# Kernel optimization log

Measured on AMD Instinct MI355X. Metric: run time of the kernel, lower is better.

The kernel has to match this reference:

```python
import jax, jax.numpy as jnp
import numpy as np

# Mamba2(d_model=256, headdim=32) defaults: d_state=128, d_conv=4, expand=2, ngroups=1, chunk=256
B, CIN, L = 8, 256, 1024
D_MODEL = CIN
D_INNER = 2 * D_MODEL            # expand=2 -> 512
HEADDIM = 32
NHEADS = D_INNER // HEADDIM      # 16
D_STATE = 128
D_CONV = 4
CONV_DIM = D_INNER + 2 * D_STATE             # 768 (ngroups=1)
D_IN_PROJ = 2 * D_INNER + 2 * D_STATE + NHEADS  # 1296
GN_GROUPS = 8
CHUNK = 256
EPS = 1e-5

def setup_inputs():
    key = jax.random.key(0)
    ks = jax.random.split(key, 8)
    x = jax.random.normal(ks[0], (B, CIN, L), jnp.float32)
    W_in = jax.random.normal(ks[1], (D_IN_PROJ, D_MODEL), jnp.float32) * 0.02
    conv_w = jax.random.normal(ks[2], (CONV_DIM, D_CONV), jnp.float32) * 0.2
    conv_b = jax.random.normal(ks[3], (CONV_DIM,), jnp.float32) * 0.02
    dt = jnp.exp(jax.random.uniform(ks[4], (NHEADS,)) * (jnp.log(0.1) - jnp.log(0.001)) + jnp.log(0.001))
    dt_bias = dt + jnp.log(-jnp.expm1(-dt))   # inverse softplus
    A_log = jnp.log(jax.random.uniform(ks[5], (NHEADS,), minval=1.0, maxval=16.0))
    Dp = jnp.ones((NHEADS,), jnp.float32)
    rms_w = jnp.ones((D_INNER,), jnp.float32)
    W_out = jax.random.normal(ks[6], (D_MODEL, D_INNER), jnp.float32) * 0.02
    gn_w = jnp.ones((CIN,), jnp.float32)
    gn_b = jnp.zeros((CIN,), jnp.float32)
    return dict(x=x, W_in=W_in, conv_w=conv_w, conv_b=conv_b, dt_bias=dt_bias,
                A_log=A_log, Dp=Dp, rms_w=rms_w, W_out=W_out, gn_w=gn_w, gn_b=gn_b)

def segsum(a):
    # a: (..., T) -> (..., T, T) with sum_{j<i<=t} a_i on/below diagonal, -inf above
    T = a.shape[-1]
    cs = jnp.cumsum(a, -1)
    d = cs[..., :, None] - cs[..., None, :]
    mask = jnp.tril(jnp.ones((T, T), bool))
    return jnp.where(mask, d, -jnp.inf)

def ssd(X, A, Bm, Cm):
    # X: (b,l,h,p) already dt-scaled; A: (b,l,h) = dt*A_cont; Bm,Cm: (b,l,n) (ngroups=1)
    b, l, h, p = X.shape
    n = Bm.shape[-1]
    c = l // CHUNK
    X = X.reshape(b, c, CHUNK, h, p)
    A = A.reshape(b, c, CHUNK, h).transpose(0, 3, 1, 2)      # (b,h,c,l)
    Bm = Bm.reshape(b, c, CHUNK, n)
    Cm = Cm.reshape(b, c, CHUNK, n)
    A_cs = jnp.cumsum(A, -1)                                  # (b,h,c,l)
    Lmat = jnp.exp(segsum(A))                                 # (b,h,c,l,l)
    Y_diag = jnp.einsum('bcln,bcsn,bhcls,bcshp->bclhp', Cm, Bm, Lmat, X)
    decay_states = jnp.exp(A_cs[..., -1:] - A_cs)             # (b,h,c,l)
    states = jnp.einsum('bcln,bhcl,bclhp->bchpn', Bm, decay_states, X)
    decay_chunk = jnp.exp(segsum(jnp.pad(A_cs[..., -1], ((0, 0), (0, 0), (1, 0)))))  # (b,h,c+1,c+1)
    states = jnp.concatenate([jnp.zeros_like(states[:, :1]), states], axis=1)        # (b,c+1,h,p,n)
    prev = jnp.einsum('bhzc,bchpn->bzhpn', decay_chunk, states)[:, :-1]              # (b,c,h,p,n)
    Y_off = jnp.einsum('bcln,bchpn,bhcl->bclhp', Cm, prev, jnp.exp(A_cs))
    return (Y_diag + Y_off).reshape(b, l, h, p)

def _forward(x, W_in, conv_w, conv_b, dt_bias, A_log, Dp, rms_w, W_out, gn_w, gn_b):
    u = jnp.transpose(x, (0, 2, 1))                           # (B,L,d_model)
    zxbcdt = u @ W_in.T                                       # (B,L,1296)
    z = zxbcdt[..., :D_INNER]
    xBC = zxbcdt[..., D_INNER:D_INNER + CONV_DIM]
    dt = jax.nn.softplus(zxbcdt[..., D_INNER + CONV_DIM:] + dt_bias)  # (B,L,H)
    # causal depthwise conv1d + SiLU
    xpad = jnp.pad(xBC, ((0, 0), (D_CONV - 1, 0), (0, 0)))
    xconv = conv_b + sum(conv_w[:, k] * xpad[:, k:k + L, :] for k in range(D_CONV))
    xconv = jax.nn.silu(xconv)
    xs = xconv[..., :D_INNER].reshape(B, L, NHEADS, HEADDIM)
    Bm = xconv[..., D_INNER:D_INNER + D_STATE]
    Cm = xconv[..., D_INNER + D_STATE:]
    A = -jnp.exp(A_log)                                       # (H,)
    Y = ssd(dt[..., None] * xs, dt * A, Bm, Cm)               # (B,L,H,P)
    Y = Y + xs * Dp[None, None, :, None]
    # gated RMSNorm (norm_before_gate=False): rmsnorm(y * silu(z)) * weight
    y = Y.reshape(B, L, D_INNER) * jax.nn.silu(z)
    y = y * jax.lax.rsqrt(jnp.mean(y * y, -1, keepdims=True) + EPS) * rms_w
    out = jnp.transpose(y @ W_out.T, (0, 2, 1))               # (B,C,L)
    # GroupNorm(8, C) over (channels_per_group, L)
    og = out.reshape(B, GN_GROUPS, CIN // GN_GROUPS, L)
    mu = og.mean((2, 3), keepdims=True)
    var = og.var((2, 3), keepdims=True)
    out = ((og - mu) * jax.lax.rsqrt(var + EPS)).reshape(B, CIN, L)
    out = out * gn_w[None, :, None] + gn_b[None, :, None]
    return out * jnp.tanh(jax.nn.softplus(out))               # Mish

def reference(x, W_in, conv_w, conv_b, dt_bias, A_log, Dp, rms_w, W_out, gn_w, gn_b):
    return _forward(x, W_in, conv_w, conv_b, dt_bias, A_log, Dp, rms_w, W_out, gn_w, gn_b)
```

## Files before the change

### kernel.cpp

```cpp
#include <hip/hip_runtime.h>
#include <hip/hip_bf16.h>
#include <math.h>

#define B_ 8
#define L_ 1024
#define DM 256
#define DI 512
#define HD 32
#define NH 16
#define DS 128
#define CDIM 768
#define NZX 1280
#define CH 256
#define NC 4
#define M_ (B_*L_)
#define EPSV 1e-5f

typedef short bf16x8 __attribute__((ext_vector_type(8)));
typedef float f32x4 __attribute__((ext_vector_type(4)));

#define OFF_ZX   0
#define SZ_ZX    (M_*NZX/2)
#define OFF_XC   (OFF_ZX+SZ_ZX)
#define SZ_XC    (M_*CDIM/2)
#define OFF_DTP  (OFF_XC+SZ_XC)
#define SZ_DTP   (4*M_*NH)
#define OFF_ACS  (OFF_DTP+SZ_DTP)
#define SZ_ACS   (B_*NC*NH*CH)
#define OFF_S0   (OFF_ACS+SZ_ACS)
#define SZ_S0    (B_*NC*CH*CH/2)
#define OFF_ST   (OFF_S0+SZ_S0)
#define SZ_ST    (B_*NC*NH*HD*DS/2)
#define OFF_Y    (OFF_ST+SZ_ST)
#define SZ_Y     (M_*DI/2)
#define OFF_YNB  (OFF_Y+SZ_Y)
#define SZ_YNB   (M_*DI/2)
#define OFF_XBF  (OFF_YNB+SZ_YNB)
#define SZ_XBF   (M_*DM/2)
#define OFF_WBF  (OFF_XBF+SZ_XBF)
#define SZ_WBF   (1296*DM/2)
#define OFF_WOBF (OFF_WBF+SZ_WBF)
#define SZ_WOBF  (DM*DI/2)
#define OFF_GNP  (OFF_WOBF+SZ_WOBF)
#define SZ_GNP   (64*2)
#define OFF_BT   (OFF_GNP+SZ_GNP)
#define SZ_BT    (32*128*256/2)
#define OFF_OUTB (OFF_BT+SZ_BT)
#define SZ_OUTB  (M_*DM/2)

__device__ __forceinline__ ushort f2bf(float v) {
  __hip_bfloat16 h = __float2bfloat16(v);
  return *(ushort*)&h;
}
__device__ __forceinline__ float bf2f(ushort u) {
  return __uint_as_float(((unsigned int)u) << 16);
}
__device__ __forceinline__ float dt_load(const float* __restrict__ dtp, size_t di) {
  float s = dtp[di] + dtp[(size_t)M_*NH + di] + dtp[2*(size_t)M_*NH + di] + dtp[3*(size_t)M_*NH + di];
  return (s > 20.f) ? s : log1pf(expf(s));
}

__device__ __forceinline__ void gload16(const ushort* g, ushort* l) {
  __builtin_amdgcn_global_load_lds(
      (const __attribute__((address_space(1))) unsigned int*)g,
      (__attribute__((address_space(3))) unsigned int*)l,
      16, 0, 0);
}

__global__ __launch_bounds__(256) void k_prep(const float* __restrict__ x,
                                              const float* __restrict__ W_in,
                                              const float* __restrict__ W_out,
                                              const float* __restrict__ dt_bias,
                                              ushort* __restrict__ xbf,
                                              ushort* __restrict__ wbf,
                                              ushort* __restrict__ wobf,
                                              float2* __restrict__ gnp,
                                              float* __restrict__ dtp) {
  __shared__ float Ts[64][65];
  __shared__ float Wd[16][65];
  const int bid = blockIdx.x;
  const int t = threadIdx.x;
  if (bid < 512) {
    const int kt = bid & 3, lt2 = (bid >> 2) & 15, b = bid >> 6;
    const int k0 = kt*64, l0 = lt2*64;
    for (int i = t; i < 1024; i += 256) {
      int kk = i>>4, lw = i&15;
      float4 v = *(const float4*)&x[(size_t)b*DM*L_ + (size_t)(k0+kk)*L_ + l0 + lw*4];
      Ts[kk][lw*4+0] = v.x; Ts[kk][lw*4+1] = v.y;
      Ts[kk][lw*4+2] = v.z; Ts[kk][lw*4+3] = v.w;
    }
    for (int i = t; i < 1024; i += 256) {
      int h = i>>6, kk = i&63;
      Wd[h][kk] = W_in[(size_t)(NZX+h)*DM + k0+kk];
    }
    __syncthreads();
    for (int i = t; i < 512; i += 256) {
      int mm = i>>3, kg = i&7;
      union { ushort u[8]; uint4 q; } pk;
#pragma unroll
      for (int j = 0; j < 8; ++j) pk.u[j] = f2bf(Ts[kg*8+j][mm]);
      *(uint4*)&xbf[(size_t)(b*L_ + l0+mm)*DM + k0 + kg*8] = pk.q;
    }
    const int h = t&15, lg = t>>4;
    const float bias = (kt == 0) ? dt_bias[h] : 0.f;
#pragma unroll
    for (int c = 0; c < 4; ++c) {
      const int ll = lg + c*16;
      float acc = bias;
#pragma unroll 8
      for (int kk = 0; kk < 64; ++kk) acc += Wd[h][kk]*Ts[kk][ll];
      dtp[(size_t)kt*M_*NH + (size_t)(b*L_ + l0+ll)*NH + h] = acc;
    }
  } else if (bid < 512 + 1296) {
    int i = (bid-512)*256 + t;
    if (i < 1296*DM) wbf[i] = f2bf(W_in[i]);
  } else if (bid < 512 + 1296 + 512) {
    int i = (bid-512-1296)*256 + t;
    wobf[i] = f2bf(W_out[i]);
  } else {
    if (t < 64) gnp[t] = make_float2(0.f, 0.f);
  }
}

__global__ __launch_bounds__(256) void k_gemm_in_mfma(const ushort* __restrict__ xbf,
                                                      const ushort* __restrict__ wbf,
                                                      ushort* __restrict__ zxb) {
  __shared__ __attribute__((aligned(16))) ushort As[2][128*32];
  __shared__ __attribute__((aligned(16))) ushort Bs[2][128*32];
  const int tid = threadIdx.x;
  const int n0 = blockIdx.x*128, m0 = blockIdx.y*128;
  const int wave = tid>>6, lane = tid&63;
  const int lr = lane&15, quad = lane>>4;
  const int rA = lane>>2;
  const int cA = (lane&3)*8;
  f32x4 acc[2][8];
#pragma unroll
  for (int mi=0;mi<2;++mi)
#pragma unroll
    for (int ni=0;ni<8;++ni)
#pragma unroll
      for (int r=0;r<4;++r) acc[mi][ni][r] = 0.f;
  auto STAGE = [&](int buf, int k0) {
#pragma unroll
    for (int j = 0; j < 2; ++j) {
      const int ch = 2*wave + j;
      const int row = ch*16 + rA;
      gload16(xbf + (size_t)(m0+row)*DM + k0 + cA, &As[buf][ch*512]);
      gload16(wbf + (size_t)(n0+row)*DM + k0 + cA, &Bs[buf][ch*512]);
    }
  };
  STAGE(0, 0);
#pragma unroll
  for (int i = 0; i < 8; ++i) {
    __syncthreads();
    if (i < 7) STAGE((i+1)&1, (i+1)*32);
    const int cur = i&1;
    bf16x8 af[2], bfr[8];
    af[0] = *(const bf16x8*)&As[cur][(wave*32+lr)*32 + quad*8];
    af[1] = *(const bf16x8*)&As[cur][(wave*32+16+lr)*32 + quad*8];
#pragma unroll
    for (int ni=0;ni<8;++ni) bfr[ni] = *(const bf16x8*)&Bs[cur][(ni*16+lr)*32 + quad*8];
#pragma unroll
    for (int mi=0;mi<2;++mi)
#pragma unroll
      for (int ni=0;ni<8;++ni)
        acc[mi][ni] = __builtin_amdgcn_mfma_f32_16x16x32_bf16(af[mi], bfr[ni], acc[mi][ni], 0, 0, 0);
  }
#pragma unroll
  for (int mi=0;mi<2;++mi) {
    int m = m0 + wave*32 + mi*16 + quad*4;
#pragma unroll
    for (int ni=0;ni<8;++ni) {
      int n = n0 + ni*16 + lr;
#pragma unroll
      for (int r=0;r<4;++r) zxb[(size_t)(m+r)*NZX + n] = f2bf(acc[mi][ni][r]);
    }
  }
}

__global__ __launch_bounds__(256) void k_conv(const ushort* __restrict__ zxb,
                                              const float* __restrict__ cw,
                                              const float* __restrict__ cb,
                                              ushort* __restrict__ xcb,
                                              ushort* __restrict__ btg) {
  const int j = blockIdx.x*256 + threadIdx.x;
  const int m8 = blockIdx.y*8;
  const int l0 = m8 & 1023;
  const int mb = m8 & ~1023;
  const float4 w = *(const float4*)&cw[j*4];
  const float bias = cb[j];
  float v[11];
#pragma unroll
  for (int i = 0; i < 11; ++i) {
    int ll = l0 - 3 + i;
    v[i] = (ll >= 0) ? bf2f(zxb[(size_t)(mb+ll)*NZX + DI + j]) : 0.f;
  }
  union { ushort u[8]; uint4 q; } res;
#pragma unroll
  for (int i = 0; i < 8; ++i) {
    float a = bias + w.x*v[i] + w.y*v[i+1] + w.z*v[i+2] + w.w*v[i+3];
    a = a / (1.f + expf(-a));
    res.u[i] = f2bf(a);
    xcb[(size_t)(mb+l0+i)*CDIM + j] = res.u[i];
  }
  if (j >= DI && j < DI+DS) {
    const int n = j - DI;
    const int bc = (mb >> 10)*NC + (l0 >> 8);
    const int lc = l0 & 255;
    *(uint4*)&btg[((size_t)bc*DS + n)*CH + lc] = res.q;
  }
}

__global__ __launch_bounds__(256) void k_s0st(const ushort* __restrict__ xcb,
                                              const ushort* __restrict__ btg,
                                              const float* __restrict__ dtp,
                                              const float* __restrict__ A_log,
                                              float* __restrict__ acs_g,
                                              ushort* __restrict__ stb,
                                              ushort* __restrict__ S0b) {
  __shared__ float wtot[4];
  __shared__ ushort Xw[32][264];
  const int role = blockIdx.x;
  const int bc = blockIdx.y;
  const int base = bc*CH;
  const int t = threadIdx.x;
  const int wave = t>>6, lane = t&63, lr = lane&15, quad = lane>>4;
  if (role < 10) {
    const int lt = (role>=6) ? 3 : (role>=3) ? 2 : (role>=1) ? 1 : 0;
    const int st = role - lt*(lt+1)/2;
    const int l = lt*64 + wave*16 + lr;
    f32x4 acc[4];
#pragma unroll
    for (int nt = 0; nt < 4; ++nt)
#pragma unroll
      for (int r = 0; r < 4; ++r) acc[nt][r] = 0.f;
#pragma unroll
    for (int ks = 0; ks < 4; ++ks) {
      bf16x8 af = *(const bf16x8*)(xcb + (size_t)(base+l)*CDIM + (DI+DS) + ks*32 + quad*8);
#pragma unroll
      for (int nt = 0; nt < 4; ++nt) {
        bf16x8 bf = *(const bf16x8*)(xcb + (size_t)(base + st*64 + nt*16 + lr)*CDIM + DI + ks*32 + quad*8);
        acc[nt] = __builtin_amdgcn_mfma_f32_16x16x32_bf16(af, bf, acc[nt], 0, 0, 0);
      }
    }
    const bool diag = (lt == st);
#pragma unroll
    for (int nt = 0; nt < 4; ++nt)
#pragma unroll
      for (int r = 0; r < 4; ++r) {
        const int lrow = lt*64 + wave*16 + quad*4 + r;
        const int scol = st*64 + nt*16 + lr;
        ushort v = (!diag || scol <= lrow) ? f2bf(acc[nt][r]) : (ushort)0;
        S0b[((size_t)bc*CH + lrow)*CH + scol] = v;
      }
    return;
  }
  const int h = role - 10;
  float dt_t = dt_load(dtp, (size_t)(base+t)*NH + h);
  float An = -expf(A_log[h]);
  float v = dt_t * An;
#pragma unroll
  for (int off = 1; off < 64; off <<= 1) {
    float u = __shfl_up(v, off);
    if (lane >= off) v += u;
  }
  if (lane == 63) wtot[wave] = v;
  __syncthreads();
  float pre = 0.f, tot = 0.f;
#pragma unroll
  for (int wj = 0; wj < 4; ++wj) {
    float wv = wtot[wj];
    tot += wv;
    if (wj < wave) pre += wv;
  }
  const float a = v + pre;
  const float alast = tot;
  acs_g[((size_t)bc*NH + h)*CH + t] = a;
  float w = expf(alast - a) * dt_t;
  {
    const ushort* xp = xcb + (size_t)(base+t)*CDIM + h*HD;
    ushort tmp[32];
    *(uint4*)&tmp[0]  = *(const uint4*)(xp);
    *(uint4*)&tmp[8]  = *(const uint4*)(xp+8);
    *(uint4*)&tmp[16] = *(const uint4*)(xp+16);
    *(uint4*)&tmp[24] = *(const uint4*)(xp+24);
#pragma unroll
    for (int p = 0; p < 32; ++p) Xw[p][t] = f2bf(bf2f(tmp[p]) * w);
  }
  __syncthreads();
  f32x4 acc2[2][2];
#pragma unroll
  for (int mt=0;mt<2;++mt)
#pragma unroll
    for (int nt=0;nt<2;++nt)
#pragma unroll
      for (int r=0;r<4;++r) acc2[mt][nt][r] = 0.f;
  const ushort* bp = btg + (size_t)bc*DS*CH;
#pragma unroll
  for (int k0 = 0; k0 < CH; k0 += 32) {
    bf16x8 a0 = *(const bf16x8*)&Xw[lr][k0 + quad*8];
    bf16x8 a1 = *(const bf16x8*)&Xw[16+lr][k0 + quad*8];
    bf16x8 b0 = *(const bf16x8*)(bp + (size_t)(wave*32 + lr)*CH + k0 + quad*8);
    bf16x8 b1 = *(const bf16x8*)(bp + (size_t)(wave*32 + 16 + lr)*CH + k0 + quad*8);
    acc2[0][0] = __builtin_amdgcn_mfma_f32_16x16x32_bf16(a0, b0, acc2[0][0], 0,0,0);
    acc2[0][1] = __builtin_amdgcn_mfma_f32_16x16x32_bf16(a0, b1, acc2[0][1], 0,0,0);
    acc2[1][0] = __builtin_amdgcn_mfma_f32_16x16x32_bf16(a1, b0, acc2[1][0], 0,0,0);
    acc2[1][1] = __builtin_amdgcn_mfma_f32_16x16x32_bf16(a1, b1, acc2[1][1], 0,0,0);
  }
  size_t sb = ((size_t)bc*NH + h)*HD*DS;
#pragma unroll
  for (int mt = 0; mt < 2; ++mt)
#pragma unroll
    for (int nt = 0; nt < 2; ++nt)
#pragma unroll
      for (int r = 0; r < 4; ++r)
        stb[sb + (size_t)(mt*16 + quad*4 + r)*DS + wave*32 + nt*16 + lr] = f2bf(acc2[mt][nt][r]);
}

__global__ __launch_bounds__(256) void k_y_mfma(const ushort* __restrict__ xcb,
    const float* __restrict__ dtp, const float* __restrict__ acs_g,
    const ushort* __restrict__ S0b, const ushort* __restrict__ stb,
    const float* __restrict__ Dp, ushort* __restrict__ Yb) {
  __shared__ ushort Xt[32][280];
  __shared__ ushort Xs[32][280];
  __shared__ float acs[CH];
  const int t = threadIdx.x;
  const int bc = blockIdx.x, h = blockIdx.y;
  const int base = bc*CH;
  const int cc = bc & 3, bc4 = bc & ~3;
  acs[t] = acs_g[((size_t)bc*NH + h)*CH + t];
  const float dts_t = dt_load(dtp, (size_t)(base+t)*NH + h);
  ushort tmp[32];
  {
    const ushort* xp = xcb + (size_t)(base+t)*CDIM + h*HD;
    *(uint4*)&tmp[0]  = *(const uint4*)(xp);
    *(uint4*)&tmp[8]  = *(const uint4*)(xp+8);
    *(uint4*)&tmp[16] = *(const uint4*)(xp+16);
    *(uint4*)&tmp[24] = *(const uint4*)(xp+24);
#pragma unroll
    for (int p = 0; p < 32; ++p) Xt[p][t] = tmp[p];
  }
  __syncthreads();
  const float e32 = expf(acs[t & ~31] - acs[t]) * dts_t;
#pragma unroll
  for (int p = 0; p < 32; ++p) Xs[p][t] = f2bf(bf2f(tmp[p]) * e32);
  __syncthreads();
  const int wave = t>>6, lane = t&63, lr = lane&15, quad = lane>>4;
  f32x4 acc[4][2];
#pragma unroll
  for (int mt=0;mt<4;++mt)
#pragma unroll
    for (int nt=0;nt<2;++nt)
#pragma unroll
      for (int r=0;r<4;++r) acc[mt][nt][r] = 0.f;
  if (cc > 0) {
    float fj[3];
    {
      float cum = 0.f;
      for (int j = cc-1; j >= 0; --j) {
        fj[j] = expf(cum);
        cum += acs_g[((size_t)(bc4+j)*NH + h)*CH + (CH-1)];
      }
    }
#pragma unroll
    for (int ks = 0; ks < 4; ++ks) {
      bf16x8 bfr[2];
#pragma unroll
      for (int nt = 0; nt < 2; ++nt) {
        float P[8];
#pragma unroll
        for (int jj = 0; jj < 8; ++jj) P[jj] = 0.f;
        for (int j = 0; j < cc; ++j) {
          bf16x8 sv = *(const bf16x8*)(stb + ((size_t)(bc4+j)*NH + h)*HD*DS
                                       + (size_t)(nt*16+lr)*DS + ks*32 + quad*8);
#pragma unroll
          for (int jj = 0; jj < 8; ++jj) P[jj] += fj[j]*bf2f((ushort)sv[jj]);
        }
        bf16x8 bb;
#pragma unroll
        for (int jj = 0; jj < 8; ++jj) bb[jj] = (short)f2bf(P[jj]);
        bfr[nt] = bb;
      }
#pragma unroll
      for (int mt = 0; mt < 4; ++mt) {
        int l = mt*64 + wave*16 + lr;
        bf16x8 af = *(const bf16x8*)(xcb + (size_t)(base+l)*CDIM + (DI+DS) + ks*32 + quad*8);
        acc[mt][0] = __builtin_amdgcn_mfma_f32_16x16x32_bf16(af, bfr[0], acc[mt][0], 0,0,0);
        acc[mt][1] = __builtin_amdgcn_mfma_f32_16x16x32_bf16(af, bfr[1], acc[mt][1], 0,0,0);
      }
    }
    const float es0 = expf(acs[0]);
#pragma unroll
    for (int mt = 0; mt < 4; ++mt)
#pragma unroll
      for (int nt = 0; nt < 2; ++nt)
#pragma unroll
        for (int r = 0; r < 4; ++r) acc[mt][nt][r] *= es0;
  }
  const int Kw = (12 + wave) >> 1;
  for (int ks = 0; ks <= Kw; ++ks) {
    const int sq = ks*32;
    const bf16x8 xb0 = *(const bf16x8*)&Xs[lr][sq + quad*8];
    const bf16x8 xb1 = *(const bf16x8*)&Xs[16+lr][sq + quad*8];
    const float g = (ks > 0) ? expf(acs[sq] - acs[sq-32]) : 1.f;
#pragma unroll
    for (int mt = 0; mt < 4; ++mt) {
      const int rt = 4*mt + wave;
      if (ks > (rt>>1)) continue;
      if (ks > 0) {
#pragma unroll
        for (int r = 0; r < 4; ++r) { acc[mt][0][r] *= g; acc[mt][1][r] *= g; }
      }
      const int l = mt*64 + wave*16 + lr;
      const bf16x8 sb = *(const bf16x8*)(S0b + ((size_t)bc*CH + l)*CH + sq + quad*8);
      acc[mt][0] = __builtin_amdgcn_mfma_f32_16x16x32_bf16(sb, xb0, acc[mt][0], 0,0,0);
      acc[mt][1] = __builtin_amdgcn_mfma_f32_16x16x32_bf16(sb, xb1, acc[mt][1], 0,0,0);
    }
  }
  const float dph = Dp[h];
#pragma unroll
  for (int mt = 0; mt < 4; ++mt) {
    const int Kmt = (4*mt + wave) >> 1;
    const float aref = acs[32*Kmt];
    const int lb = mt*64 + wave*16 + quad*4;
#pragma unroll
    for (int r = 0; r < 4; ++r) {
      const float e = expf(acs[lb+r] - aref);
#pragma unroll
      for (int nt = 0; nt < 2; ++nt) {
        const int p = nt*16 + lr;
        float xv = bf2f(Xt[p][lb+r]);
        Yb[(size_t)(base+lb+r)*DI + h*HD + p] = f2bf(acc[mt][nt][r]*e + dph*xv);
      }
    }
  }
}

__global__ __launch_bounds__(256) void k_rms(const ushort* __restrict__ zxb,
                                             const ushort* __restrict__ Yb,
                                             const float* __restrict__ rw,
                                             ushort* __restrict__ yn) {
  const int m = blockIdx.x*4 + (threadIdx.x>>6);
  const int lane = threadIdx.x & 63;
  const int c0 = lane*8;
  bf16x8 zv = *(const bf16x8*)(zxb + (size_t)m*NZX + c0);
  bf16x8 yv = *(const bf16x8*)(Yb  + (size_t)m*DI  + c0);
  float y[8];
  float ss = 0.f;
#pragma unroll
  for (int j = 0; j < 8; ++j) {
    float z = bf2f((ushort)zv[j]);
    y[j] = bf2f((ushort)yv[j]) * z / (1.f + expf(-z));
    ss += y[j]*y[j];
  }
#pragma unroll
  for (int off = 1; off < 64; off <<= 1) ss += __shfl_xor(ss, off);
  const float inv = rsqrtf(ss * (1.f/DI) + EPSV);
  float4 w0 = *(const float4*)&rw[c0];
  float4 w1 = *(const float4*)&rw[c0+4];
  const float wv[8] = {w0.x,w0.y,w0.z,w0.w,w1.x,w1.y,w1.z,w1.w};
  union { ushort u[8]; uint4 q; } pk;
#pragma unroll
  for (int j = 0; j < 8; ++j) pk.u[j] = f2bf(y[j] * inv * wv[j]);
  *(uint4*)(yn + (size_t)m*DI + c0) = pk.q;
}

__global__ __launch_bounds__(256) void k_gemm_out_mfma(const ushort* __restrict__ ynbf,
                                                       const ushort* __restrict__ wobf,
                                                       ushort* __restrict__ outb,
                                                       float2* __restrict__ gnp) {
  __shared__ __attribute__((aligned(16))) ushort As[2][64*64];
  __shared__ __attribute__((aligned(16))) ushort Bs[2][64*64];
  const int tid = threadIdx.x;
  const int n0 = blockIdx.x*64, m0 = blockIdx.y*64;
  const int wave = tid>>6, lane = tid&63;
  const int lr = lane&15, quad = lane>>4;
  const int rA = lane>>3;
  const int cA = ((lane&7) ^ rA)*8;
  f32x4 acc[2][2];
#pragma unroll
  for (int mi=0;mi<2;++mi)
#pragma unroll
    for (int ni=0;ni<2;++ni)
#pragma unroll
      for (int r=0;r<4;++r) acc[mi][ni][r] = 0.f;
  auto STAGE = [&](int buf, int k0) {
#pragma unroll
    for (int j = 0; j < 2; ++j) {
      const int ch = 2*wave + j;
      const int row = ch*8 + rA;
      gload16(ynbf + (size_t)(m0+row)*DI + k0 + cA, &As[buf][ch*512]);
      gload16(wobf + (size_t)(n0+row)*DI + k0 + cA, &Bs[buf][ch*512]);
    }
  };
  STAGE(0, 0);
  const int mw = wave>>1, nw = wave&1;
#pragma unroll
  for (int i = 0; i < 8; ++i) {
    __syncthreads();
    if (i < 7) STAGE((i+1)&1, (i+1)*64);
    const int cur = i&1;
#pragma unroll
    for (int ks = 0; ks < 2; ++ks) {
      bf16x8 af[2], bfr[2];
#pragma unroll
      for (int mi = 0; mi < 2; ++mi) {
        const int R = mw*32 + mi*16 + lr;
        af[mi] = *(const bf16x8*)&As[cur][R*64 + (((ks*4+quad) ^ (R&7))*8)];
      }
#pragma unroll
      for (int ni = 0; ni < 2; ++ni) {
        const int R = nw*32 + ni*16 + lr;
        bfr[ni] = *(const bf16x8*)&Bs[cur][R*64 + (((ks*4+quad) ^ (R&7))*8)];
      }
#pragma unroll
      for (int mi=0;mi<2;++mi)
#pragma unroll
        for (int ni=0;ni<2;++ni)
          acc[mi][ni] = __builtin_amdgcn_mfma_f32_16x16x32_bf16(af[mi], bfr[ni], acc[mi][ni], 0, 0, 0);
    }
  }
  const int b = m0 >> 10, l0 = m0 & 1023;
  float sg = 0.f, sq2 = 0.f;
#pragma unroll
  for (int mi=0;mi<2;++mi)
#pragma unroll
    for (int ni=0;ni<2;++ni) {
      const int n = n0 + nw*32 + ni*16 + lr;
      union { ushort u[4]; uint2 q; } pk;
#pragma unroll
      for (int r=0;r<4;++r) {
        const float v = acc[mi][ni][r];
        pk.u[r] = f2bf(v);
        sg += v; sq2 += v*v;
      }
      *(uint2*)&outb[(size_t)b*DM*L_ + (size_t)n*L_ + l0 + mw*32 + mi*16 + quad*4] = pk.q;
    }
#pragma unroll
  for (int off = 32; off > 0; off >>= 1) {
    sg  += __shfl_down(sg,  off);
    sq2 += __shfl_down(sq2, off);
  }
  if (lane == 0) {
    const int gi = b*8 + (n0>>5) + nw;
    atomicAdd(&gnp[gi].x, sg);
    atomicAdd(&gnp[gi].y, sq2);
  }
}

__global__ __launch_bounds__(256) void k_gn_apply(const float2* __restrict__ gnp,
                                                  const float* __restrict__ gw,
                                                  const float* __restrict__ gb,
                                                  const ushort* __restrict__ ob,
                                                  float* __restrict__ o) {
  const int ch = blockIdx.x & 255, b = blockIdx.x >> 8;
  const int t = threadIdx.x;
  float2 p = gnp[b*8 + (ch>>5)];
  const float mean = p.x * (1.f/(32.f*L_));
  const float var  = p.y * (1.f/(32.f*L_)) - mean*mean;
  const float inv  = rsqrtf(var + EPSV);
  const float w = gw[ch], bb = gb[ch];
  size_t base = (size_t)blockIdx.x * L_;
  ushort4 v = *(const ushort4*)&ob[base + t*4];
  float r[4] = {bf2f(v.x), bf2f(v.y), bf2f(v.z), bf2f(v.w)};
#pragma unroll
  for (int j = 0; j < 4; ++j) {
    float u = (r[j] - mean) * inv * w + bb;
    float m;
    if (u > 15.f) m = u;
    else {
      float e = expf(u);
      float a = 1.f + e;
      float a2 = a*a;
      m = u * (a2 - 1.f) / (a2 + 1.f);
    }
    r[j] = m;
  }
  *(float4*)&o[base + t*4] = make_float4(r[0], r[1], r[2], r[3]);
}

extern "C" void kernel_launch(void* const* d_in, const int* in_sizes, int n_in,
                              void* d_out, int out_size, void* d_ws, size_t ws_size,
                              hipStream_t stream) {
  const float* x       = (const float*)d_in[0];
  const float* W_in    = (const float*)d_in[1];
  const float* conv_w  = (const float*)d_in[2];
  const float* conv_b  = (const float*)d_in[3];
  const float* dt_bias = (const float*)d_in[4];
  const float* A_log   = (const float*)d_in[5];
  const float* Dp      = (const float*)d_in[6];
  const float* rms_w   = (const float*)d_in[7];
  const float* W_out   = (const float*)d_in[8];
  const float* gn_w    = (const float*)d_in[9];
  const float* gn_b    = (const float*)d_in[10];
  float* out = (float*)d_out;
  float* ws  = (float*)d_ws;

  ushort* zxb   = (ushort*)(ws + OFF_ZX);
  ushort* xcb   = (ushort*)(ws + OFF_XC);
  float*  dtp   = ws + OFF_DTP;
  float*  acs   = ws + OFF_ACS;
  ushort* S0b   = (ushort*)(ws + OFF_S0);
  ushort* stb   = (ushort*)(ws + OFF_ST);
  ushort* Ybb   = (ushort*)(ws + OFF_Y);
  ushort* ynbf  = (ushort*)(ws + OFF_YNB);
  ushort* xbf   = (ushort*)(ws + OFF_XBF);
  ushort* wbf   = (ushort*)(ws + OFF_WBF);
  ushort* wobf  = (ushort*)(ws + OFF_WOBF);
  float2* gnp   = (float2*)(ws + OFF_GNP);
  ushort* btg   = (ushort*)(ws + OFF_BT);
  ushort* outb  = (ushort*)(ws + OFF_OUTB);

  k_prep         <<<dim3(512+1296+512+1), 256, 0, stream>>>(x, W_in, W_out, dt_bias,
                                                            xbf, wbf, wobf, gnp, dtp);
  k_gemm_in_mfma <<<dim3(NZX/128, M_/128), 256, 0, stream>>>(xbf, wbf, zxb);
  k_conv         <<<dim3(3, M_/8), 256, 0, stream>>>(zxb, conv_w, conv_b, xcb, btg);
  k_s0st         <<<dim3(26, B_*NC), 256, 0, stream>>>(xcb, btg, dtp, A_log, acs, stb, S0b);
  k_y_mfma       <<<dim3(B_*NC, NH), 256, 0, stream>>>(xcb, dtp, acs, S0b, stb, Dp, Ybb);
  k_rms          <<<dim3(M_/4), 256, 0, stream>>>(zxb, Ybb, rms_w, ynbf);
  k_gemm_out_mfma<<<dim3(DM/64, M_/64), 256, 0, stream>>>(ynbf, wobf, outb, gnp);
  k_gn_apply     <<<dim3(B_*DM), 256, 0, stream>>>(gnp, gn_w, gn_b, outb, out);
}
```

Before: 179.4 us.

## Fuse all stages into a persistent megakernel with grid-wide atomic barriers

Replaces the eight separate kernel launches with one persistent kernel of 256 blocks that loops over each stage's work items and separates stages with atomic-counter grid barriers, plus a tiny init kernel that zeroes the barrier counters and the GroupNorm accumulators. Shared memory becomes a union across stages. Weight conversion is also vectorized to 8 elements per thread. This targets launch overhead and the tail gaps between kernels, but the fixed grid may underuse the GPU in the large stages, and the barriers rely on all blocks being co-resident.

Measured after the change: 421.9 us. 135% more time.

```diff
diff --git a/kernel.cpp b/kernel.cpp
--- a/kernel.cpp
+++ b/kernel.cpp
@@ -15,6 +15,7 @@
 #define NC 4
 #define M_ (B_*L_)
 #define EPSV 1e-5f
+#define GRID 256
 
 typedef short bf16x8 __attribute__((ext_vector_type(8)));
 typedef float f32x4 __attribute__((ext_vector_type(4)));
@@ -47,6 +48,7 @@
 #define SZ_BT    (32*128*256/2)
 #define OFF_OUTB (OFF_BT+SZ_BT)
 #define SZ_OUTB  (M_*DM/2)
+#define OFF_BAR  (OFF_OUTB+SZ_OUTB)
 
 __device__ __forceinline__ ushort f2bf(float v) {
   __hip_bfloat16 h = __float2bfloat16(v);
@@ -59,7 +61,6 @@
   float s = dtp[di] + dtp[(size_t)M_*NH + di] + dtp[2*(size_t)M_*NH + di] + dtp[3*(size_t)M_*NH + di];
   return (s > 20.f) ? s : log1pf(expf(s));
 }
-
 __device__ __forceinline__ void gload16(const ushort* g, ushort* l) {
   __builtin_amdgcn_global_load_lds(
       (const __attribute__((address_space(1))) unsigned int*)g,
@@ -67,516 +68,519 @@
       16, 0, 0);
 }
 
-__global__ __launch_bounds__(256) void k_prep(const float* __restrict__ x,
-                                              const float* __restrict__ W_in,
-                                              const float* __restrict__ W_out,
-                                              const float* __restrict__ dt_bias,
-                                              ushort* __restrict__ xbf,
-                                              ushort* __restrict__ wbf,
-                                              ushort* __restrict__ wobf,
-                                              float2* __restrict__ gnp,
-                                              float* __restrict__ dtp) {
-  __shared__ float Ts[64][65];
-  __shared__ float Wd[16][65];
-  const int bid = blockIdx.x;
+__device__ __forceinline__ void gbar(int* ctr) {
+  __syncthreads();
+  if (threadIdx.x == 0) {
+    __hip_atomic_fetch_add(ctr, 1, __ATOMIC_ACQ_REL, __HIP_MEMORY_SCOPE_AGENT);
+    while (__hip_atomic_load(ctr, __ATOMIC_ACQUIRE, __HIP_MEMORY_SCOPE_AGENT) < GRID)
+      __builtin_amdgcn_s_sleep(2);
+  }
+  __syncthreads();
+}
+
+union SMem {
+  struct { float Ts[64][65]; float Wd[16][65]; } prep;
+  struct { ushort As[2][128*32]; ushort Bs[2][128*32]; } gin;
+  struct { float wtot[4]; ushort Xw[32][264]; } s0;
+  struct { ushort Xt[32][280]; ushort Xs[32][280]; float acs[CH]; } y;
+  struct { ushort As[2][64*64]; ushort Bs[2][64*64]; } gout;
+};
+
+__global__ __launch_bounds__(256) void k_init(float2* __restrict__ gnp, int* __restrict__ bar) {
   const int t = threadIdx.x;
-  if (bid < 512) {
-    const int kt = bid & 3, lt2 = (bid >> 2) & 15, b = bid >> 6;
-    const int k0 = kt*64, l0 = lt2*64;
-    for (int i = t; i < 1024; i += 256) {
-      int kk = i>>4, lw = i&15;
-      float4 v = *(const float4*)&x[(size_t)b*DM*L_ + (size_t)(k0+kk)*L_ + l0 + lw*4];
-      Ts[kk][lw*4+0] = v.x; Ts[kk][lw*4+1] = v.y;
-      Ts[kk][lw*4+2] = v.z; Ts[kk][lw*4+3] = v.w;
-    }
-    for (int i = t; i < 1024; i += 256) {
-      int h = i>>6, kk = i&63;
-      Wd[h][kk] = W_in[(size_t)(NZX+h)*DM + k0+kk];
-    }
-    __syncthreads();
-    for (int i = t; i < 512; i += 256) {
-      int mm = i>>3, kg = i&7;
-      union { ushort u[8]; uint4 q; } pk;
-#pragma unroll
-      for (int j = 0; j < 8; ++j) pk.u[j] = f2bf(Ts[kg*8+j][mm]);
-      *(uint4*)&xbf[(size_t)(b*L_ + l0+mm)*DM + k0 + kg*8] = pk.q;
-    }
-    const int h = t&15, lg = t>>4;
-    const float bias = (kt == 0) ? dt_bias[h] : 0.f;
-#pragma unroll
-    for (int c = 0; c < 4; ++c) {
-      const int ll = lg + c*16;
-      float acc = bias;
-#pragma unroll 8
-      for (int kk = 0; kk < 64; ++kk) acc += Wd[h][kk]*Ts[kk][ll];
-      dtp[(size_t)kt*M_*NH + (size_t)(b*L_ + l0+ll)*NH + h] = acc;
-    }
-  } else if (bid < 512 + 1296) {
-    int i = (bid-512)*256 + t;
-    if (i < 1296*DM) wbf[i] = f2bf(W_in[i]);
-  } else if (bid < 512 + 1296 + 512) {
-    int i = (bid-512-1296)*256 + t;
-    wobf[i] = f2bf(W_out[i]);
-  } else {
-    if (t < 64) gnp[t] = make_float2(0.f, 0.f);
-  }
-}
-
-__global__ __launch_bounds__(256) void k_gemm_in_mfma(const ushort* __restrict__ xbf,
-                                                      const ushort* __restrict__ wbf,
-                                                      ushort* __restrict__ zxb) {
-  __shared__ __attribute__((aligned(16))) ushort As[2][128*32];
-  __shared__ __attribute__((aligned(16))) ushort Bs[2][128*32];
-  const int tid = threadIdx.x;
-  const int n0 = blockIdx.x*128, m0 = blockIdx.y*128;
-  const int wave = tid>>6, lane = tid&63;
-  const int lr = lane&15, quad = lane>>4;
-  const int rA = lane>>2;
-  const int cA = (lane&3)*8;
-  f32x4 acc[2][8];
-#pragma unroll
-  for (int mi=0;mi<2;++mi)
-#pragma unroll
-    for (int ni=0;ni<8;++ni)
-#pragma unroll
-      for (int r=0;r<4;++r) acc[mi][ni][r] = 0.f;
-  auto STAGE = [&](int buf, int k0) {
-#pragma unroll
-    for (int j = 0; j < 2; ++j) {
-      const int ch = 2*wave + j;
-      const int row = ch*16 + rA;
-      gload16(xbf + (size_t)(m0+row)*DM + k0 + cA, &As[buf][ch*512]);
-      gload16(wbf + (size_t)(n0+row)*DM + k0 + cA, &Bs[buf][ch*512]);
-    }
-  };
-  STAGE(0, 0);
-#pragma unroll
-  for (int i = 0; i < 8; ++i) {
-    __syncthreads();
-    if (i < 7) STAGE((i+1)&1, (i+1)*32);
-    const int cur = i&1;
-    bf16x8 af[2], bfr[8];
-    af[0] = *(const bf16x8*)&As[cur][(wave*32+lr)*32 + quad*8];
-    af[1] = *(const bf16x8*)&As[cur][(wave*32+16+lr)*32 + quad*8];
-#pragma unroll
-    for (int ni=0;ni<8;++ni) bfr[ni] = *(const bf16x8*)&Bs[cur][(ni*16+lr)*32 + quad*8];
-#pragma unroll
-    for (int mi=0;mi<2;++mi)
-#pragma unroll
-      for (int ni=0;ni<8;++ni)
-        acc[mi][ni] = __builtin_amdgcn_mfma_f32_16x16x32_bf16(af[mi], bfr[ni], acc[mi][ni], 0, 0, 0);
-  }
-#pragma unroll
-  for (int mi=0;mi<2;++mi) {
-    int m = m0 + wave*32 + mi*16 + quad*4;
-#pragma unroll
-    for (int ni=0;ni<8;++ni) {
-      int n = n0 + ni*16 + lr;
-#pragma unroll
-      for (int r=0;r<4;++r) zxb[(size_t)(m+r)*NZX + n] = f2bf(acc[mi][ni][r]);
-    }
-  }
-}
-
-__global__ __launch_bounds__(256) void k_conv(const ushort* __restrict__ zxb,
-                                              const float* __restrict__ cw,
-                                              const float* __restrict__ cb,
-                                              ushort* __restrict__ xcb,
-                                              ushort* __restrict__ btg) {
-  const int j = blockIdx.x*256 + threadIdx.x;
-  const int m8 = blockIdx.y*8;
-  const int l0 = m8 & 1023;
-  const int mb = m8 & ~1023;
-  const float4 w = *(const float4*)&cw[j*4];
-  const float bias = cb[j];
-  float v[11];
-#pragma unroll
-  for (int i = 0; i < 11; ++i) {
-    int ll = l0 - 3 + i;
-    v[i] = (ll >= 0) ? bf2f(zxb[(size_t)(mb+ll)*NZX + DI + j]) : 0.f;
-  }
-  union { ushort u[8]; uint4 q; } res;
-#pragma unroll
-  for (int i = 0; i < 8; ++i) {
-    float a = bias + w.x*v[i] + w.y*v[i+1] + w.z*v[i+2] + w.w*v[i+3];
-    a = a / (1.f + expf(-a));
-    res.u[i] = f2bf(a);
-    xcb[(size_t)(mb+l0+i)*CDIM + j] = res.u[i];
-  }
-  if (j >= DI && j < DI+DS) {
-    const int n = j - DI;
-    const int bc = (mb >> 10)*NC + (l0 >> 8);
-    const int lc = l0 & 255;
-    *(uint4*)&btg[((size_t)bc*DS + n)*CH + lc] = res.q;
-  }
-}
-
-__global__ __launch_bounds__(256) void k_s0st(const ushort* __restrict__ xcb,
-                                              const ushort* __restrict__ btg,
-                                              const float* __restrict__ dtp,
-                                              const float* __restrict__ A_log,
-                                              float* __restrict__ acs_g,
-                                              ushort* __restrict__ stb,
-                                              ushort* __restrict__ S0b) {
-  __shared__ float wtot[4];
-  __shared__ ushort Xw[32][264];
-  const int role = blockIdx.x;
-  const int bc = blockIdx.y;
-  const int base = bc*CH;
+  if (t < 64) gnp[t] = make_float2(0.f, 0.f);
+  if (t < 8)  bar[t] = 0;
+}
+
+__global__ __launch_bounds__(256, 2) void k_mega(
+    const float* __restrict__ x, const float* __restrict__ W_in,
+    const float* __restrict__ conv_w, const float* __restrict__ conv_b,
+    const float* __restrict__ dt_bias, const float* __restrict__ A_log,
+    const float* __restrict__ Dp, const float* __restrict__ rms_w,
+    const float* __restrict__ W_out, const float* __restrict__ gn_w,
+    const float* __restrict__ gn_b, float* __restrict__ out,
+    ushort* __restrict__ xbf, ushort* __restrict__ wbf, ushort* __restrict__ wobf,
+    float2* __restrict__ gnp, float* __restrict__ dtp,
+    ushort* __restrict__ zxb, ushort* __restrict__ xcb, ushort* __restrict__ btg,
+    float* __restrict__ acs_g, ushort* __restrict__ S0b, ushort* __restrict__ stb,
+    ushort* __restrict__ Yb, ushort* __restrict__ ynbf, ushort* __restrict__ outb,
+    int* __restrict__ bar) {
+  __shared__ SMem sm;
   const int t = threadIdx.x;
   const int wave = t>>6, lane = t&63, lr = lane&15, quad = lane>>4;
-  if (role < 10) {
-    const int lt = (role>=6) ? 3 : (role>=3) ? 2 : (role>=1) ? 1 : 0;
-    const int st = role - lt*(lt+1)/2;
-    const int l = lt*64 + wave*16 + lr;
-    f32x4 acc[4];
-#pragma unroll
-    for (int nt = 0; nt < 4; ++nt)
-#pragma unroll
-      for (int r = 0; r < 4; ++r) acc[nt][r] = 0.f;
-#pragma unroll
-    for (int ks = 0; ks < 4; ++ks) {
-      bf16x8 af = *(const bf16x8*)(xcb + (size_t)(base+l)*CDIM + (DI+DS) + ks*32 + quad*8);
-#pragma unroll
-      for (int nt = 0; nt < 4; ++nt) {
-        bf16x8 bf = *(const bf16x8*)(xcb + (size_t)(base + st*64 + nt*16 + lr)*CDIM + DI + ks*32 + quad*8);
-        acc[nt] = __builtin_amdgcn_mfma_f32_16x16x32_bf16(af, bf, acc[nt], 0, 0, 0);
-      }
-    }
-    const bool diag = (lt == st);
-#pragma unroll
-    for (int nt = 0; nt < 4; ++nt)
+
+  for (int bid = blockIdx.x; bid < 738; bid += GRID) {
+    if (bid < 512) {
+      const int kt = bid & 3, lt2 = (bid >> 2) & 15, b = bid >> 6;
+      const int k0 = kt*64, l0 = lt2*64;
+      for (int i = t; i < 1024; i += 256) {
+        int kk = i>>4, lw = i&15;
+        float4 v = *(const float4*)&x[(size_t)b*DM*L_ + (size_t)(k0+kk)*L_ + l0 + lw*4];
+        sm.prep.Ts[kk][lw*4+0] = v.x; sm.prep.Ts[kk][lw*4+1] = v.y;
+        sm.prep.Ts[kk][lw*4+2] = v.z; sm.prep.Ts[kk][lw*4+3] = v.w;
+      }
+      for (int i = t; i < 1024; i += 256) {
+        int hh = i>>6, kk = i&63;
+        sm.prep.Wd[hh][kk] = W_in[(size_t)(NZX+hh)*DM + k0+kk];
+      }
+      __syncthreads();
+      for (int i = t; i < 512; i += 256) {
+        int mm = i>>3, kg = i&7;
+        union { ushort u[8]; uint4 q; } pk;
+#pragma unroll
+        for (int j = 0; j < 8; ++j) pk.u[j] = f2bf(sm.prep.Ts[kg*8+j][mm]);
+        *(uint4*)&xbf[(size_t)(b*L_ + l0+mm)*DM + k0 + kg*8] = pk.q;
+      }
+      const int hh = t&15, lg = t>>4;
+      const float bias = (kt == 0) ? dt_bias[hh] : 0.f;
+#pragma unroll
+      for (int c = 0; c < 4; ++c) {
+        const int ll = lg + c*16;
+        float acc = bias;
+#pragma unroll 8
+        for (int kk = 0; kk < 64; ++kk) acc += sm.prep.Wd[hh][kk]*sm.prep.Ts[kk][ll];
+        dtp[(size_t)kt*M_*NH + (size_t)(b*L_ + l0+ll)*NH + hh] = acc;
+      }
+    } else if (bid < 674) {
+      const int i = ((bid-512)*256 + t)*8;
+      float4 a = *(const float4*)&W_in[i];
+      float4 b4 = *(const float4*)&W_in[i+4];
+      union { ushort u[8]; uint4 q; } pk;
+      pk.u[0]=f2bf(a.x); pk.u[1]=f2bf(a.y); pk.u[2]=f2bf(a.z); pk.u[3]=f2bf(a.w);
+      pk.u[4]=f2bf(b4.x); pk.u[5]=f2bf(b4.y); pk.u[6]=f2bf(b4.z); pk.u[7]=f2bf(b4.w);
+      *(uint4*)&wbf[i] = pk.q;
+    } else {
+      const int i = ((bid-674)*256 + t)*8;
+      float4 a = *(const float4*)&W_out[i];
+      float4 b4 = *(const float4*)&W_out[i+4];
+      union { ushort u[8]; uint4 q; } pk;
+      pk.u[0]=f2bf(a.x); pk.u[1]=f2bf(a.y); pk.u[2]=f2bf(a.z); pk.u[3]=f2bf(a.w);
+      pk.u[4]=f2bf(b4.x); pk.u[5]=f2bf(b4.y); pk.u[6]=f2bf(b4.z); pk.u[7]=f2bf(b4.w);
+      *(uint4*)&wobf[i] = pk.q;
+    }
+    __syncthreads();
+  }
+  gbar(&bar[0]);
+
+  for (int bid = blockIdx.x; bid < 640; bid += GRID) {
+    const int n0 = (bid%10)*128, m0 = (bid/10)*128;
+    const int rA = lane>>2, cA = (lane&3)*8;
+    f32x4 acc[2][8];
+#pragma unroll
+    for (int mi=0;mi<2;++mi)
+#pragma unroll
+      for (int ni=0;ni<8;++ni)
+#pragma unroll
+        for (int r=0;r<4;++r) acc[mi][ni][r] = 0.f;
+    auto STAGE = [&](int buf, int k0) {
+#pragma unroll
+      for (int j = 0; j < 2; ++j) {
+        const int ch = 2*wave + j;
+        const int row = ch*16 + rA;
+        gload16(xbf + (size_t)(m0+row)*DM + k0 + cA, &sm.gin.As[buf][ch*512]);
+        gload16(wbf + (size_t)(n0+row)*DM + k0 + cA, &sm.gin.Bs[buf][ch*512]);
+      }
+    };
+    STAGE(0, 0);
+#pragma unroll
+    for (int i = 0; i < 8; ++i) {
+      __syncthreads();
+      if (i < 7) STAGE((i+1)&1, (i+1)*32);
+      const int cur = i&1;
+      bf16x8 af[2], bfr[8];
+      af[0] = *(const bf16x8*)&sm.gin.As[cur][(wave*32+lr)*32 + quad*8];
+      af[1] = *(const bf16x8*)&sm.gin.As[cur][(wave*32+16+lr)*32 + quad*8];
+#pragma unroll
+      for (int ni=0;ni<8;++ni) bfr[ni] = *(const bf16x8*)&sm.gin.Bs[cur][(ni*16+lr)*32 + quad*8];
+#pragma unroll
+      for (int mi=0;mi<2;++mi)
+#pragma unroll
+        for (int ni=0;ni<8;++ni)
+          acc[mi][ni] = __builtin_amdgcn_mfma_f32_16x16x32_bf16(af[mi], bfr[ni], acc[mi][ni], 0, 0, 0);
+    }
+#pragma unroll
+    for (int mi=0;mi<2;++mi) {
+      int m = m0 + wave*32 + mi*16 + quad*4;
+#pragma unroll
+      for (int ni=0;ni<8;++ni) {
+        int n = n0 + ni*16 + lr;
+#pragma unroll
+        for (int r=0;r<4;++r) zxb[(size_t)(m+r)*NZX + n] = f2bf(acc[mi][ni][r]);
+      }
+    }
+    __syncthreads();
+  }
+  gbar(&bar[1]);
+
+  for (int bid = blockIdx.x; bid < 3072; bid += GRID) {
+    const int j = (bid%3)*256 + t;
+    const int m8 = (bid/3)*8;
+    const int l0 = m8 & 1023;
+    const int mb = m8 & ~1023;
+    const float4 w = *(const float4*)&conv_w[j*4];
+    const float bias = conv_b[j];
+    float v[11];
+#pragma unroll
+    for (int i = 0; i < 11; ++i) {
+      int ll = l0 - 3 + i;
+      v[i] = (ll >= 0) ? bf2f(zxb[(size_t)(mb+ll)*NZX + DI + j]) : 0.f;
+    }
+    union { ushort u[8]; uint4 q; } res;
+#pragma unroll
+    for (int i = 0; i < 8; ++i) {
+      float a = bias + w.x*v[i] + w.y*v[i+1] + w.z*v[i+2] + w.w*v[i+3];
+      a = a / (1.f + expf(-a));
+      res.u[i] = f2bf(a);
+      xcb[(size_t)(mb+l0+i)*CDIM + j] = res.u[i];
+    }
+    if (j >= DI && j < DI+DS) {
+      const int n = j - DI;
+      const int bc = (mb >> 10)*NC + (l0 >> 8);
+      const int lc = l0 & 255;
+      *(uint4*)&btg[((size_t)bc*DS + n)*CH + lc] = res.q;
+    }
+  }
+  gbar(&bar[2]);
+
+  for (int bid = blockIdx.x; bid < 832; bid += GRID) {
+    const int role = bid % 26;
+    const int bc = bid / 26;
+    const int base = bc*CH;
+    if (role < 10) {
+      const int lt = (role>=6) ? 3 : (role>=3) ? 2 : (role>=1) ? 1 : 0;
+      const int st = role - lt*(lt+1)/2;
+      const int l = lt*64 + wave*16 + lr;
+      f32x4 acc[4];
+#pragma unroll
+      for (int nt = 0; nt < 4; ++nt)
+#pragma unroll
+        for (int r = 0; r < 4; ++r) acc[nt][r] = 0.f;
+#pragma unroll
+      for (int ks = 0; ks < 4; ++ks) {
+        bf16x8 af = *(const bf16x8*)(xcb + (size_t)(base+l)*CDIM + (DI+DS) + ks*32 + quad*8);
+#pragma unroll
+        for (int nt = 0; nt < 4; ++nt) {
+          bf16x8 bf = *(const bf16x8*)(xcb + (size_t)(base + st*64 + nt*16 + lr)*CDIM + DI + ks*32 + quad*8);
+          acc[nt] = __builtin_amdgcn_mfma_f32_16x16x32_bf16(af, bf, acc[nt], 0, 0, 0);
+        }
+      }
+      const bool diag = (lt == st);
+#pragma unroll
+      for (int nt = 0; nt < 4; ++nt)
+#pragma unroll
+        for (int r = 0; r < 4; ++r) {
+          const int lrow = lt*64 + wave*16 + quad*4 + r;
+          const int scol = st*64 + nt*16 + lr;
+          ushort v = (!diag || scol <= lrow) ? f2bf(acc[nt][r]) : (ushort)0;
+          S0b[((size_t)bc*CH + lrow)*CH + scol] = v;
+        }
+    } else {
+      const int h = role - 10;
+      float dt_t = dt_load(dtp, (size_t)(base+t)*NH + h);
+      float An = -expf(A_log[h]);
+      float v = dt_t * An;
+#pragma unroll
+      for (int off = 1; off < 64; off <<= 1) {
+        float u = __shfl_up(v, off);
+        if (lane >= off) v += u;
+      }
+      if (lane == 63) sm.s0.wtot[wave] = v;
+      __syncthreads();
+      float pre = 0.f, tot = 0.f;
+#pragma unroll
+      for (int wj = 0; wj < 4; ++wj) {
+        float wv = sm.s0.wtot[wj];
+        tot += wv;
+        if (wj < wave) pre += wv;
+      }
+      const float a = v + pre;
+      const float alast = tot;
+      acs_g[((size_t)bc*NH + h)*CH + t] = a;
+      float w = expf(alast - a) * dt_t;
+      {
+        const ushort* xp = xcb + (size_t)(base+t)*CDIM + h*HD;
+        ushort tmp[32];
+        *(uint4*)&tmp[0]  = *(const uint4*)(xp);
+        *(uint4*)&tmp[8]  = *(const uint4*)(xp+8);
+        *(uint4*)&tmp[16] = *(const uint4*)(xp+16);
+        *(uint4*)&tmp[24] = *(const uint4*)(xp+24);
+#pragma unroll
+        for (int p = 0; p < 32; ++p) sm.s0.Xw[p][t] = f2bf(bf2f(tmp[p]) * w);
+      }
+      __syncthreads();
+      f32x4 acc2[2][2];
+#pragma unroll
+      for (int mt=0;mt<2;++mt)
+#pragma unroll
+        for (int nt=0;nt<2;++nt)
+#pragma unroll
+          for (int r=0;r<4;++r) acc2[mt][nt][r] = 0.f;
+      const ushort* bp = btg + (size_t)bc*DS*CH;
+#pragma unroll
+      for (int k0 = 0; k0 < CH; k0 += 32) {
+        bf16x8 a0 = *(const bf16x8*)&sm.s0.Xw[lr][k0 + quad*8];
+        bf16x8 a1 = *(const bf16x8*)&sm.s0.Xw[16+lr][k0 + quad*8];
+        bf16x8 b0 = *(const bf16x8*)(bp + (size_t)(wave*32 + lr)*CH + k0 + quad*8);
+        bf16x8 b1 = *(const bf16x8*)(bp + (size_t)(wave*32 + 16 + lr)*CH + k0 + quad*8);
+        acc2[0][0] = __builtin_amdgcn_mfma_f32_16x16x32_bf16(a0, b0, acc2[0][0], 0,0,0);
+        acc2[0][1] = __builtin_amdgcn_mfma_f32_16x16x32_bf16(a0, b1, acc2[0][1], 0,0,0);
+        acc2[1][0] = __builtin_amdgcn_mfma_f32_16x16x32_bf16(a1, b0, acc2[1][0], 0,0,0);
+        acc2[1][1] = __builtin_amdgcn_mfma_f32_16x16x32_bf16(a1, b1, acc2[1][1], 0,0,0);
+      }
+      size_t sb = ((size_t)bc*NH + h)*HD*DS;
+#pragma unroll
+      for (int mt = 0; mt < 2; ++mt)
+#pragma unroll
+        for (int nt = 0; nt < 2; ++nt)
+#pragma unroll
+          for (int r = 0; r < 4; ++r)
+            stb[sb + (size_t)(mt*16 + quad*4 + r)*DS + wave*32 + nt*16 + lr] = f2bf(acc2[mt][nt][r]);
+    }
+    __syncthreads();
+  }
+  gbar(&bar[3]);
+
+  for (int bid = blockIdx.x; bid < 512; bid += GRID) {
+    const int bc = bid & 31, h = bid >> 5;
+    const int base = bc*CH;
+    const int cc = bc & 3, bc4 = bc & ~3;
+    sm.y.acs[t] = acs_g[((size_t)bc*NH + h)*CH + t];
+    const float dts_t = dt_load(dtp, (size_t)(base+t)*NH + h);
+    ushort tmp[32];
+    {
+      const ushort* xp = xcb + (size_t)(base+t)*CDIM + h*HD;
+      *(uint4*)&tmp[0]  = *(const uint4*)(xp);
+      *(uint4*)&tmp[8]  = *(const uint4*)(xp+8);
+      *(uint4*)&tmp[16] = *(const uint4*)(xp+16);
+      *(uint4*)&tmp[24] = *(const uint4*)(xp+24);
+#pragma unroll
+      for (int p = 0; p < 32; ++p) sm.y.Xt[p][t] = tmp[p];
+    }
+    __syncthreads();
+    const float e32 = expf(sm.y.acs[t & ~31] - sm.y.acs[t]) * dts_t;
+#pragma unroll
+    for (int p = 0; p < 32; ++p) sm.y.Xs[p][t] = f2bf(bf2f(tmp[p]) * e32);
+    __syncthreads();
+    f32x4 acc[4][2];
+#pragma unroll
+    for (int mt=0;mt<4;++mt)
+#pragma unroll
+      for (int nt=0;nt<2;++nt)
+#pragma unroll
+        for (int r=0;r<4;++r) acc[mt][nt][r] = 0.f;
+    if (cc > 0) {
+      float fj[3];
+      {
+        float cum = 0.f;
+        for (int j = cc-1; j >= 0; --j) {
+          fj[j] = expf(cum);
+          cum += acs_g[((size_t)(bc4+j)*NH + h)*CH + (CH-1)];
+        }
+      }
+#pragma unroll
+      for (int ks = 0; ks < 4; ++ks) {
+        bf16x8 bfr[2];
+#pragma unroll
+        for (int nt = 0; nt < 2; ++nt) {
+          float P[8];
+#pragma unroll
+          for (int jj = 0; jj < 8; ++jj) P[jj] = 0.f;
+          for (int j = 0; j < cc; ++j) {
+            bf16x8 sv = *(const bf16x8*)(stb + ((size_t)(bc4+j)*NH + h)*HD*DS
+                                         + (size_t)(nt*16+lr)*DS + ks*32 + quad*8);
+#pragma unroll
+            for (int jj = 0; jj < 8; ++jj) P[jj] += fj[j]*bf2f((ushort)sv[jj]);
+          }
+          bf16x8 bb;
+#pragma unroll
+          for (int jj = 0; jj < 8; ++jj) bb[jj] = (short)f2bf(P[jj]);
+          bfr[nt] = bb;
+        }
+#pragma unroll
+        for (int mt = 0; mt < 4; ++mt) {
+          int l = mt*64 + wave*16 + lr;
+          bf16x8 af = *(const bf16x8*)(xcb + (size_t)(base+l)*CDIM + (DI+DS) + ks*32 + quad*8);
+          acc[mt][0] = __builtin_amdgcn_mfma_f32_16x16x32_bf16(af, bfr[0], acc[mt][0], 0,0,0);
+          acc[mt][1] = __builtin_amdgcn_mfma_f32_16x16x32_bf16(af, bfr[1], acc[mt][1], 0,0,0);
+        }
+      }
+      const float es0 = expf(sm.y.acs[0]);
+#pragma unroll
+      for (int mt = 0; mt < 4; ++mt)
+#pragma unroll
+        for (int nt = 0; nt < 2; ++nt)
+#pragma unroll
+          for (int r = 0; r < 4; ++r) acc[mt][nt][r] *= es0;
+    }
+    const int Kw = (12 + wave) >> 1;
+    for (int ks = 0; ks <= Kw; ++ks) {
+      const int sq = ks*32;
+      const bf16x8 xb0 = *(const bf16x8*)&sm.y.Xs[lr][sq + quad*8];
+      const bf16x8 xb1 = *(const bf16x8*)&sm.y.Xs[16+lr][sq + quad*8];
+      const float g = (ks > 0) ? expf(sm.y.acs[sq] - sm.y.acs[sq-32]) : 1.f;
+#pragma unroll
+      for (int mt = 0; mt < 4; ++mt) {
+        const int rt = 4*mt + wave;
+        if (ks > (rt>>1)) continue;
+        if (ks > 0) {
+#pragma unroll
+          for (int r = 0; r < 4; ++r) { acc[mt][0][r] *= g; acc[mt][1][r] *= g; }
+        }
+        const int l = mt*64 + wave*16 + lr;
+        const bf16x8 sb = *(const bf16x8*)(S0b + ((size_t)bc*CH + l)*CH + sq + quad*8);
+        acc[mt][0] = __builtin_amdgcn_mfma_f32_16x16x32_bf16(sb, xb0, acc[mt][0], 0,0,0);
+        acc[mt][1] = __builtin_amdgcn_mfma_f32_16x16x32_bf16(sb, xb1, acc[mt][1], 0,0,0);
+      }
+    }
+    const float dph = Dp[h];
+#pragma unroll
+    for (int mt = 0; mt < 4; ++mt) {
+      const int Kmt = (4*mt + wave) >> 1;
+      const float aref = sm.y.acs[32*Kmt];
+      const int lb = mt*64 + wave*16 + quad*4;
 #pragma unroll
       for (int r = 0; r < 4; ++r) {
-        const int lrow = lt*64 + wave*16 + quad*4 + r;
-        const int scol = st*64 + nt*16 + lr;
-        ushort v = (!diag || scol <= lrow) ? f2bf(acc[nt][r]) : (ushort)0;
-        S0b[((size_t)bc*CH + lrow)*CH + scol] = v;
-      }
-    return;
-  }
-  const int h = role - 10;
-  float dt_t = dt_load(dtp, (size_t)(base+t)*NH + h);
-  float An = -expf(A_log[h]);
-  float v = dt_t * An;
-#pragma unroll
-  for (int off = 1; off < 64; off <<= 1) {
-    float u = __shfl_up(v, off);
-    if (lane >= off) v += u;
-  }
-  if (lane == 63) wtot[wave] = v;
-  __syncthreads();
-  float pre = 0.f, tot = 0.f;
-#pragma unroll
-  for (int wj = 0; wj < 4; ++wj) {
-    float wv = wtot[wj];
-    tot += wv;
-    if (wj < wave) pre += wv;
-  }
-  const float a = v + pre;
-  const float alast = tot;
-  acs_g[((size_t)bc*NH + h)*CH + t] = a;
-  float w = expf(alast - a) * dt_t;
-  {
-    const ushort* xp = xcb + (size_t)(base+t)*CDIM + h*HD;
-    ushort tmp[32];
-    *(uint4*)&tmp[0]  = *(const uint4*)(xp);
-    *(uint4*)&tmp[8]  = *(const uint4*)(xp+8);
-    *(uint4*)&tmp[16] = *(const uint4*)(xp+16);
-    *(uint4*)&tmp[24] = *(const uint4*)(xp+24);
-#pragma unroll
-    for (int p = 0; p < 32; ++p) Xw[p][t] = f2bf(bf2f(tmp[p]) * w);
-  }
-  __syncthreads();
-  f32x4 acc2[2][2];
-#pragma unroll
-  for (int mt=0;mt<2;++mt)
-#pragma unroll
-    for (int nt=0;nt<2;++nt)
-#pragma unroll
-      for (int r=0;r<4;++r) acc2[mt][nt][r] = 0.f;
-  const ushort* bp = btg + (size_t)bc*DS*CH;
-#pragma unroll
-  for (int k0 = 0; k0 < CH; k0 += 32) {
-    bf16x8 a0 = *(const bf16x8*)&Xw[lr][k0 + quad*8];
-    bf16x8 a1 = *(const bf16x8*)&Xw[16+lr][k0 + quad*8];
-    bf16x8 b0 = *(const bf16x8*)(bp + (size_t)(wave*32 + lr)*CH + k0 + quad*8);
-    bf16x8 b1 = *(const bf16x8*)(bp + (size_t)(wave*32 + 16 + lr)*CH + k0 + quad*8);
-    acc2[0][0] = __builtin_amdgcn_mfma_f32_16x16x32_bf16(a0, b0, acc2[0][0], 0,0,0);
-    acc2[0][1] = __builtin_amdgcn_mfma_f32_16x16x32_bf16(a0, b1, acc2[0][1], 0,0,0);
-    acc2[1][0] = __builtin_amdgcn_mfma_f32_16x16x32_bf16(a1, b0, acc2[1][0], 0,0,0);
-    acc2[1][1] = __builtin_amdgcn_mfma_f32_16x16x32_bf16(a1, b1, acc2[1][1], 0,0,0);
-  }
-  size_t sb = ((size_t)bc*NH + h)*HD*DS;
-#pragma unroll
-  for (int mt = 0; mt < 2; ++mt)
-#pragma unroll
-    for (int nt = 0; nt < 2; ++nt)
-#pragma unroll
-      for (int r = 0; r < 4; ++r)
-        stb[sb + (size_t)(mt*16 + quad*4 + r)*DS + wave*32 + nt*16 + lr] = f2bf(acc2[mt][nt][r]);
-}
-
-__global__ __launch_bounds__(256) void k_y_mfma(const ushort* __restrict__ xcb,
-    const float* __restrict__ dtp, const float* __restrict__ acs_g,
-    const ushort* __restrict__ S0b, const ushort* __restrict__ stb,
-    const float* __restrict__ Dp, ushort* __restrict__ Yb) {
-  __shared__ ushort Xt[32][280];
-  __shared__ ushort Xs[32][280];
-  __shared__ float acs[CH];
-  const int t = threadIdx.x;
-  const int bc = blockIdx.x, h = blockIdx.y;
-  const int base = bc*CH;
-  const int cc = bc & 3, bc4 = bc & ~3;
-  acs[t] = acs_g[((size_t)bc*NH + h)*CH + t];
-  const float dts_t = dt_load(dtp, (size_t)(base+t)*NH + h);
-  ushort tmp[32];
-  {
-    const ushort* xp = xcb + (size_t)(base+t)*CDIM + h*HD;
-    *(uint4*)&tmp[0]  = *(const uint4*)(xp);
-    *(uint4*)&tmp[8]  = *(const uint4*)(xp+8);
-    *(uint4*)&tmp[16] = *(const uint4*)(xp+16);
-    *(uint4*)&tmp[24] = *(const uint4*)(xp+24);
-#pragma unroll
-    for (int p = 0; p < 32; ++p) Xt[p][t] = tmp[p];
-  }
-  __syncthreads();
-  const float e32 = expf(acs[t & ~31] - acs[t]) * dts_t;
-#pragma unroll
-  for (int p = 0; p < 32; ++p) Xs[p][t] = f2bf(bf2f(tmp[p]) * e32);
-  __syncthreads();
-  const int wave = t>>6, lane = t&63, lr = lane&15, quad = lane>>4;
-  f32x4 acc[4][2];
-#pragma unroll
-  for (int mt=0;mt<4;++mt)
-#pragma unroll
-    for (int nt=0;nt<2;++nt)
-#pragma unroll
-      for (int r=0;r<4;++r) acc[mt][nt][r] = 0.f;
-  if (cc > 0) {
-    float fj[3];
-    {
-      float cum = 0.f;
-      for (int j = cc-1; j >= 0; --j) {
-        fj[j] = expf(cum);
-        cum += acs_g[((size_t)(bc4+j)*NH + h)*CH + (CH-1)];
-      }
-    }
-#pragma unroll
-    for (int ks = 0; ks < 4; ++ks) {
-      bf16x8 bfr[2];
-#pragma unroll
-      for (int nt = 0; nt < 2; ++nt) {
-        float P[8];
-#pragma unroll
-        for (int jj = 0; jj < 8; ++jj) P[jj] = 0.f;
-        for (int j = 0; j < cc; ++j) {
-          bf16x8 sv = *(const bf16x8*)(stb + ((size_t)(bc4+j)*NH + h)*HD*DS
-                                       + (size_t)(nt*16+lr)*DS + ks*32 + quad*8);
-#pragma unroll
-          for (int jj = 0; jj < 8; ++jj) P[jj] += fj[j]*bf2f((ushort)sv[jj]);
-        }
-        bf16x8 bb;
-#pragma unroll
-        for (int jj = 0; jj < 8; ++jj) bb[jj] = (short)f2bf(P[jj]);
-        bfr[nt] = bb;
-      }
-#pragma unroll
-      for (int mt = 0; mt < 4; ++mt) {
-        int l = mt*64 + wave*16 + lr;
-        bf16x8 af = *(const bf16x8*)(xcb + (size_t)(base+l)*CDIM + (DI+DS) + ks*32 + quad*8);
-        acc[mt][0] = __builtin_amdgcn_mfma_f32_16x16x32_bf16(af, bfr[0], acc[mt][0], 0,0,0);
-        acc[mt][1] = __builtin_amdgcn_mfma_f32_16x16x32_bf16(af, bfr[1], acc[mt][1], 0,0,0);
-      }
-    }
-    const float es0 = expf(acs[0]);
-#pragma unroll
-    for (int mt = 0; mt < 4; ++mt)
-#pragma unroll
-      for (int nt = 0; nt < 2; ++nt)
-#pragma unroll
-        for (int r = 0; r < 4; ++r) acc[mt][nt][r] *= es0;
-  }
-  const int Kw = (12 + wave) >> 1;
-  for (int ks = 0; ks <= Kw; ++ks) {
-    const int sq = ks*32;
-    const bf16x8 xb0 = *(const bf16x8*)&Xs[lr][sq + quad*8];
-    const bf16x8 xb1 = *(const bf16x8*)&Xs[16+lr][sq + quad*8];
-    const float g = (ks > 0) ? expf(acs[sq] - acs[sq-32]) : 1.f;
-#pragma unroll
-    for (int mt = 0; mt < 4; ++mt) {
-      const int rt = 4*mt + wave;
-      if (ks > (rt>>1)) continue;
-      if (ks > 0) {
-#pragma unroll
-        for (int r = 0; r < 4; ++r) { acc[mt][0][r] *= g; acc[mt][1][r] *= g; }
-      }
-      const int l = mt*64 + wave*16 + lr;
-      const bf16x8 sb = *(const bf16x8*)(S0b + ((size_t)bc*CH + l)*CH + sq + quad*8);
-      acc[mt][0] = __builtin_amdgcn_mfma_f32_16x16x32_bf16(sb, xb0, acc[mt][0], 0,0,0);
-      acc[mt][1] = __builtin_amdgcn_mfma_f32_16x16x32_bf16(sb, xb1, acc[mt][1], 0,0,0);
-    }
-  }
-  const float dph = Dp[h];
-#pragma unroll
-  for (int mt = 0; mt < 4; ++mt) {
-    const int Kmt = (4*mt + wave) >> 1;
-    const float aref = acs[32*Kmt];
-    const int lb = mt*64 + wave*16 + quad*4;
-#pragma unroll
-    for (int r = 0; r < 4; ++r) {
-      const float e = expf(acs[lb+r] - aref);
-#pragma unroll
-      for (int nt = 0; nt < 2; ++nt) {
-        const int p = nt*16 + lr;
-        float xv = bf2f(Xt[p][lb+r]);
-        Yb[(size_t)(base+lb+r)*DI + h*HD + p] = f2bf(acc[mt][nt][r]*e + dph*xv);
-      }
-    }
-  }
-}
-
-__global__ __launch_bounds__(256) void k_rms(const ushort* __restrict__ zxb,
-                                             const ushort* __restrict__ Yb,
-                                             const float* __restrict__ rw,
-                                             ushort* __restrict__ yn) {
-  const int m = blockIdx.x*4 + (threadIdx.x>>6);
-  const int lane = threadIdx.x & 63;
-  const int c0 = lane*8;
-  bf16x8 zv = *(const bf16x8*)(zxb + (size_t)m*NZX + c0);
-  bf16x8 yv = *(const bf16x8*)(Yb  + (size_t)m*DI  + c0);
-  float y[8];
-  float ss = 0.f;
-#pragma unroll
-  for (int j = 0; j < 8; ++j) {
-    float z = bf2f((ushort)zv[j]);
-    y[j] = bf2f((ushort)yv[j]) * z / (1.f + expf(-z));
-    ss += y[j]*y[j];
-  }
-#pragma unroll
-  for (int off = 1; off < 64; off <<= 1) ss += __shfl_xor(ss, off);
-  const float inv = rsqrtf(ss * (1.f/DI) + EPSV);
-  float4 w0 = *(const float4*)&rw[c0];
-  float4 w1 = *(const float4*)&rw[c0+4];
-  const float wv[8] = {w0.x,w0.y,w0.z,w0.w,w1.x,w1.y,w1.z,w1.w};
-  union { ushort u[8]; uint4 q; } pk;
-#pragma unroll
-  for (int j = 0; j < 8; ++j) pk.u[j] = f2bf(y[j] * inv * wv[j]);
-  *(uint4*)(yn + (size_t)m*DI + c0) = pk.q;
-}
-
-__global__ __launch_bounds__(256) void k_gemm_out_mfma(const ushort* __restrict__ ynbf,
-                                                       const ushort* __restrict__ wobf,
-                                                       ushort* __restrict__ outb,
-                                                       float2* __restrict__ gnp) {
-  __shared__ __attribute__((aligned(16))) ushort As[2][64*64];
-  __shared__ __attribute__((aligned(16))) ushort Bs[2][64*64];
-  const int tid = threadIdx.x;
-  const int n0 = blockIdx.x*64, m0 = blockIdx.y*64;
-  const int wave = tid>>6, lane = tid&63;
-  const int lr = lane&15, quad = lane>>4;
-  const int rA = lane>>3;
-  const int cA = ((lane&7) ^ rA)*8;
-  f32x4 acc[2][2];
-#pragma unroll
-  for (int mi=0;mi<2;++mi)
-#pragma unroll
-    for (int ni=0;ni<2;++ni)
-#pragma unroll
-      for (int r=0;r<4;++r) acc[mi][ni][r] = 0.f;
-  auto STAGE = [&](int buf, int k0) {
-#pragma unroll
-    for (int j = 0; j < 2; ++j) {
-      const int ch = 2*wave + j;
-      const int row = ch*8 + rA;
-      gload16(ynbf + (size_t)(m0+row)*DI + k0 + cA, &As[buf][ch*512]);
-      gload16(wobf + (size_t)(n0+row)*DI + k0 + cA, &Bs[buf][ch*512]);
-    }
-  };
-  STAGE(0, 0);
-  const int mw = wave>>1, nw = wave&1;
-#pragma unroll
-  for (int i = 0; i < 8; ++i) {
+        const float e = expf(sm.y.acs[lb+r] - aref);
+#pragma unroll
+        for (int nt = 0; nt < 2; ++nt) {
+          const int p = nt*16 + lr;
+          float xv = bf2f(sm.y.Xt[p][lb+r]);
+          Yb[(size_t)(base+lb+r)*DI + h*HD + p] = f2bf(acc[mt][nt][r]*e + dph*xv);
+        }
+      }
+    }
     __syncthreads();
-    if (i < 7) STAGE((i+1)&1, (i+1)*64);
-    const int cur = i&1;
-#pragma unroll
-    for (int ks = 0; ks < 2; ++ks) {
-      bf16x8 af[2], bfr[2];
-#pragma unroll
-      for (int mi = 0; mi < 2; ++mi) {
-        const int R = mw*32 + mi*16 + lr;
-        af[mi] = *(const bf16x8*)&As[cur][R*64 + (((ks*4+quad) ^ (R&7))*8)];
-      }
-#pragma unroll
-      for (int ni = 0; ni < 2; ++ni) {
-        const int R = nw*32 + ni*16 + lr;
-        bfr[ni] = *(const bf16x8*)&Bs[cur][R*64 + (((ks*4+quad) ^ (R&7))*8)];
-      }
-#pragma unroll
-      for (int mi=0;mi<2;++mi)
-#pragma unroll
-        for (int ni=0;ni<2;++ni)
-          acc[mi][ni] = __builtin_amdgcn_mfma_f32_16x16x32_bf16(af[mi], bfr[ni], acc[mi][ni], 0, 0, 0);
-    }
-  }
-  const int b = m0 >> 10, l0 = m0 & 1023;
-  float sg = 0.f, sq2 = 0.f;
-#pragma unroll
-  for (int mi=0;mi<2;++mi)
-#pragma unroll
-    for (int ni=0;ni<2;++ni) {
-      const int n = n0 + nw*32 + ni*16 + lr;
-      union { ushort u[4]; uint2 q; } pk;
-#pragma unroll
-      for (int r=0;r<4;++r) {
-        const float v = acc[mi][ni][r];
-        pk.u[r] = f2bf(v);
-        sg += v; sq2 += v*v;
-      }
-      *(uint2*)&outb[(size_t)b*DM*L_ + (size_t)n*L_ + l0 + mw*32 + mi*16 + quad*4] = pk.q;
-    }
-#pragma unroll
-  for (int off = 32; off > 0; off >>= 1) {
-    sg  += __shfl_down(sg,  off);
-    sq2 += __shfl_down(sq2, off);
-  }
-  if (lane == 0) {
-    const int gi = b*8 + (n0>>5) + nw;
-    atomicAdd(&gnp[gi].x, sg);
-    atomicAdd(&gnp[gi].y, sq2);
-  }
-}
-
-__global__ __launch_bounds__(256) void k_gn_apply(const float2* __restrict__ gnp,
-                                                  const float* __restrict__ gw,
-                                                  const float* __restrict__ gb,
-                                                  const ushort* __restrict__ ob,
-                                                  float* __restrict__ o) {
-  const int ch = blockIdx.x & 255, b = blockIdx.x >> 8;
-  const int t = threadIdx.x;
-  float2 p = gnp[b*8 + (ch>>5)];
-  const float mean = p.x * (1.f/(32.f*L_));
-  const float var  = p.y * (1.f/(32.f*L_)) - mean*mean;
-  const float inv  = rsqrtf(var + EPSV);
-  const float w = gw[ch], bb = gb[ch];
-  size_t base = (size_t)blockIdx.x * L_;
-  ushort4 v = *(const ushort4*)&ob[base + t*4];
-  float r[4] = {bf2f(v.x), bf2f(v.y), bf2f(v.z), bf2f(v.w)};
-#pragma unroll
-  for (int j = 0; j < 4; ++j) {
-    float u = (r[j] - mean) * inv * w + bb;
-    float m;
-    if (u > 15.f) m = u;
-    else {
-      float e = expf(u);
-      float a = 1.f + e;
-      float a2 = a*a;
-      m = u * (a2 - 1.f) / (a2 + 1.f);
-    }
-    r[j] = m;
-  }
-  *(float4*)&o[base + t*4] = make_float4(r[0], r[1], r[2], r[3]);
+  }
+  gbar(&bar[4]);
+
+  for (int bid = blockIdx.x; bid < 2048; bid += GRID) {
+    const int m = bid*4 + wave;
+    const int c0 = lane*8;
+    bf16x8 zv = *(const bf16x8*)(zxb + (size_t)m*NZX + c0);
+    bf16x8 yv = *(const bf16x8*)(Yb  + (size_t)m*DI  + c0);
+    float y[8];
+    float ss = 0.f;
+#pragma unroll
+    for (int j = 0; j < 8; ++j) {
+      float z = bf2f((ushort)zv[j]);
+      y[j] = bf2f((ushort)yv[j]) * z / (1.f + expf(-z));
+      ss += y[j]*y[j];
+    }
+#pragma unroll
+    for (int off = 1; off < 64; off <<= 1) ss += __shfl_xor(ss, off);
+    const float inv = rsqrtf(ss * (1.f/DI) + EPSV);
+    float4 w0 = *(const float4*)&rms_w[c0];
+    float4 w1 = *(const float4*)&rms_w[c0+4];
+    const float wv[8] = {w0.x,w0.y,w0.z,w0.w,w1.x,w1.y,w1.z,w1.w};
+    union { ushort u[8]; uint4 q; } pk;
+#pragma unroll
+    for (int j = 0; j < 8; ++j) pk.u[j] = f2bf(y[j] * inv * wv[j]);
+    *(uint4*)(ynbf + (size_t)m*DI + c0) = pk.q;
+  }
+  gbar(&bar[5]);
+
+  for (int bid = blockIdx.x; bid < 512; bid += GRID) {
+    const int n0 = (bid & 3)*64, m0 = (bid >> 2)*64;
+    const int rA = lane>>3;
+    const int cA = ((lane&7) ^ rA)*8;
+    f32x4 acc[2][2];
+#pragma unroll
+    for (int mi=0;mi<2;++mi)
+#pragma unroll
+      for (int ni=0;ni<2;++ni)
+#pragma unroll
+        for (int r=0;r<4;++r) acc[mi][ni][r] = 0.f;
+    auto STAGE = [&](int buf, int k0) {
+#pragma unroll
+      for (int j = 0; j < 2; ++j) {
+        const int ch = 2*wave + j;
+        const int row = ch*8 + rA;
+        gload16(ynbf + (size_t)(m0+row)*DI + k0 + cA, &sm.gout.As[buf][ch*512]);
+        gload16(wobf + (size_t)(n0+row)*DI + k0 + cA, &sm.gout.Bs[buf][ch*512]);
+      }
+    };
+    STAGE(0, 0);
+    const int mw = wave>>1, nw = wave&1;
+#pragma unroll
+    for (int i = 0; i < 8; ++i) {
+      __syncthreads();
+      if (i < 7) STAGE((i+1)&1, (i+1)*64);
+      const int cur = i&1;
+#pragma unroll
+      for (int ks = 0; ks < 2; ++ks) {
+        bf16x8 af[2], bfr[2];
+#pragma unroll
+        for (int mi = 0; mi < 2; ++mi) {
+          const int R = mw*32 + mi*16 + lr;
+          af[mi] = *(const bf16x8*)&sm.gout.As[cur][R*64 + (((ks*4+quad) ^ (R&7))*8)];
+        }
+#pragma unroll
+        for (int ni = 0; ni < 2; ++ni) {
+          const int R = nw*32 + ni*16 + lr;
+          bfr[ni] = *(const bf16x8*)&sm.gout.Bs[cur][R*64 + (((ks*4+quad) ^ (R&7))*8)];
+        }
+#pragma unroll
+        for (int mi=0;mi<2;++mi)
+#pragma unroll
+          for (int ni=0;ni<2;++ni)
+            acc[mi][ni] = __builtin_amdgcn_mfma_f32_16x16x32_bf16(af[mi], bfr[ni], acc[mi][ni], 0, 0, 0);
+      }
+    }
+    const int b = m0 >> 10, l0 = m0 & 1023;
+    float sg = 0.f, sq2 = 0.f;
+#pragma unroll
+    for (int mi=0;mi<2;++mi)
+#pragma unroll
+      for (int ni=0;ni<2;++ni) {
+        const int n = n0 + nw*32 + ni*16 + lr;
+        union { ushort u[4]; uint2 q; } pk;
+#pragma unroll
+        for (int r=0;r<4;++r) {
+          const float v = acc[mi][ni][r];
+          pk.u[r] = f2bf(v);
+          sg += v; sq2 += v*v;
+        }
+        *(uint2*)&outb[(size_t)b*DM*L_ + (size_t)n*L_ + l0 + mw*32 + mi*16 + quad*4] = pk.q;
+      }
+#pragma unroll
+    for (int off = 32; off > 0; off >>= 1) {
+      sg  += __shfl_down(sg,  off);
+      sq2 += __shfl_down(sq2, off);
+    }
+    if (lane == 0) {
+      const int gi = b*8 + (n0>>5) + nw;
+      atomicAdd(&gnp[gi].x, sg);
+      atomicAdd(&gnp[gi].y, sq2);
+    }
+    __syncthreads();
+  }
+  gbar(&bar[6]);
+
+  for (int bid = blockIdx.x; bid < 2048; bid += GRID) {
+    const int ch = bid & 255, b = bid >> 8;
+    float2 p = gnp[b*8 + (ch>>5)];
+    const float mean = p.x * (1.f/(32.f*L_));
+    const float var  = p.y * (1.f/(32.f*L_)) - mean*mean;
+    const float inv  = rsqrtf(var + EPSV);
+    const float w = gn_w[ch], bb = gn_b[ch];
+    size_t base = (size_t)bid * L_;
+    ushort4 v = *(const ushort4*)&outb[base + t*4];
+    float r[4] = {bf2f(v.x), bf2f(v.y), bf2f(v.z), bf2f(v.w)};
+#pragma unroll
+    for (int j = 0; j < 4; ++j) {
+      float u = (r[j] - mean) * inv * w + bb;
+      float m;
+      if (u > 15.f) m = u;
+      else {
+        float e = expf(u);
+        float a = 1.f + e;
+        float a2 = a*a;
+        m = u * (a2 - 1.f) / (a2 + 1.f);
+      }
+      r[j] = m;
+    }
+    *(float4*)&out[base + t*4] = make_float4(r[0], r[1], r[2], r[3]);
+  }
 }
 
 extern "C" void kernel_launch(void* const* d_in, const int* in_sizes, int n_in,
@@ -610,14 +614,12 @@
   float2* gnp   = (float2*)(ws + OFF_GNP);
   ushort* btg   = (ushort*)(ws + OFF_BT);
   ushort* outb  = (ushort*)(ws + OFF_OUTB);
-
-  k_prep         <<<dim3(512+1296+512+1), 256, 0, stream>>>(x, W_in, W_out, dt_bias,
-                                                            xbf, wbf, wobf, gnp, dtp);
-  k_gemm_in_mfma <<<dim3(NZX/128, M_/128), 256, 0, stream>>>(xbf, wbf, zxb);
-  k_conv         <<<dim3(3, M_/8), 256, 0, stream>>>(zxb, conv_w, conv_b, xcb, btg);
-  k_s0st         <<<dim3(26, B_*NC), 256, 0, stream>>>(xcb, btg, dtp, A_log, acs, stb, S0b);
-  k_y_mfma       <<<dim3(B_*NC, NH), 256, 0, stream>>>(xcb, dtp, acs, S0b, stb, Dp, Ybb);
-  k_rms          <<<dim3(M_/4), 256, 0, stream>>>(zxb, Ybb, rms_w, ynbf);
-  k_gemm_out_mfma<<<dim3(DM/64, M_/64), 256, 0, stream>>>(ynbf, wobf, outb, gnp);
-  k_gn_apply     <<<dim3(B_*DM), 256, 0, stream>>>(gnp, gn_w, gn_b, outb, out);
-}
+  int*    bar   = (int*)(ws + OFF_BAR);
+
+  k_init<<<dim3(1), 256, 0, stream>>>(gnp, bar);
+  k_mega<<<dim3(GRID), 256, 0, stream>>>(x, W_in, conv_w, conv_b, dt_bias, A_log,
+                                         Dp, rms_w, W_out, gn_w, gn_b, out,
+                                         xbf, wbf, wobf, gnp, dtp,
+                                         zxb, xcb, btg, acs, S0b, stb,
+                                         Ybb, ynbf, outb, bar);
+}
```
